# Kernel tuning notes

Hardware: AMD Instinct MI355X
Metric: run time of the kernel (lower is better)

Reference implementation:

```python
import jax, jax.numpy as jnp
import numpy as np

B, L, DIM = 1, 2048, 4096
H, KV, HD = 32, 8, 128
REP = H // KV
SCALE = HD ** -0.5
ROPE_BASE = 10000.0


def rope_traditional(x, offset=0):
    # x: [B, H, L, D] ; traditional RoPE rotates interleaved pairs (x[2i], x[2i+1])
    D = x.shape[-1]
    Lx = x.shape[2]
    pos = jnp.arange(offset, offset + Lx, dtype=jnp.float32)            # [L]
    inv_freq = ROPE_BASE ** (-jnp.arange(0, D, 2, dtype=jnp.float32) / D)  # [D/2]
    ang = pos[:, None] * inv_freq[None, :]                               # [L, D/2]
    c, s = jnp.cos(ang), jnp.sin(ang)
    x1 = x[..., 0::2]
    x2 = x[..., 1::2]
    r1 = x1 * c - x2 * s
    r2 = x1 * s + x2 * c
    return jnp.stack([r1, r2], axis=-1).reshape(x.shape).astype(x.dtype)


def setup_inputs() -> dict:
    key = jax.random.key(0)
    k0, k1, k2, k3, k4 = jax.random.split(key, 5)
    x = jax.random.normal(k0, (B, L, DIM), dtype=jnp.float32)
    wq = jax.random.normal(k1, (DIM, H * HD), dtype=jnp.float32) * 0.02
    wk = jax.random.normal(k2, (DIM, KV * HD), dtype=jnp.float32) * 0.02
    wv = jax.random.normal(k3, (DIM, KV * HD), dtype=jnp.float32) * 0.02
    wo = jax.random.normal(k4, (H * HD, DIM), dtype=jnp.float32) * 0.02
    # additive causal mask (prefill)
    causal = jnp.tril(jnp.ones((L, L), dtype=bool))
    mask = jnp.where(causal, 0.0, -1e9).astype(jnp.float32)
    return {"x": x, "wq": wq, "wk": wk, "wv": wv, "wo": wo, "mask": mask}


def reference(x, wq, wk, wv, wo, mask):
    Bx, Lx, _ = x.shape
    q = (x @ wq).reshape(Bx, Lx, H, HD).transpose(0, 2, 1, 3)   # [B,H,L,hd]
    k = (x @ wk).reshape(Bx, Lx, KV, HD).transpose(0, 2, 1, 3)  # [B,KV,L,hd]
    v = (x @ wv).reshape(Bx, Lx, KV, HD).transpose(0, 2, 1, 3)
    # GQA head repeat (each kv head repeated REP times contiguously)
    k = jnp.repeat(k, REP, axis=1)  # [B,H,L,hd]
    v = jnp.repeat(v, REP, axis=1)
    # RoPE applied after repeat (cache=None branch), offset 0
    q = rope_traditional(q)
    k = rope_traditional(k)
    scores = jnp.einsum("bhld,bhmd->bhlm", q * SCALE, k) + mask  # [B,H,L,L]
    probs = jax.nn.softmax(scores.astype(jnp.float32), axis=-1).astype(scores.dtype)
    out = jnp.einsum("bhlm,bhmd->bhld", probs, v)
    out = out.transpose(0, 2, 1, 3).reshape(Bx, Lx, H * HD)
    return out @ wo, k, v
```

## Files before the change

kernel.cpp:

```cpp
#include <hip/hip_runtime.h>
#include <hip/hip_bf16.h>
#include <math.h>


#define L_SEQ 2048
#define DIM   4096
#define NH    32
#define NKV   8
#define HD    128
#define SCALE 0.08838834764831845f

typedef __bf16 bf16x8 __attribute__((ext_vector_type(8)));
typedef __bf16 bf16x4 __attribute__((ext_vector_type(4)));
typedef __bf16 bf16x2 __attribute__((ext_vector_type(2)));
typedef float  f32x4  __attribute__((ext_vector_type(4)));

__device__ __forceinline__ void gld16(const void* g, void* l) {
  __builtin_amdgcn_global_load_lds(
      (const __attribute__((address_space(1))) void*)g,
      (__attribute__((address_space(3))) void*)l, 16, 0, 0);
}

__global__ void cast_bf16_kernel(const float* __restrict__ in,
                                 __bf16* __restrict__ out, long n4) {
  long i = blockIdx.x * (long)blockDim.x + threadIdx.x;
  if (i >= n4) return;
  float4 f = reinterpret_cast<const float4*>(in)[i];
  bf16x4 o;
  o[0] = (__bf16)f.x; o[1] = (__bf16)f.y; o[2] = (__bf16)f.z; o[3] = (__bf16)f.w;
  reinterpret_cast<bf16x4*>(out)[i] = o;
}

__global__ void tcast_kernel(const float* __restrict__ in0, __bf16* __restrict__ out0,
                             const float* __restrict__ in1, __bf16* __restrict__ out1,
                             int K, int N) {
  __shared__ float tile[32][33];
  const float* in  = blockIdx.z ? in1  : in0;
  __bf16*     out  = blockIdx.z ? out1 : out0;
  int n0 = blockIdx.x * 32, k0 = blockIdx.y * 32;
  int tx = threadIdx.x & 31, ty = threadIdx.x >> 5;
#pragma unroll
  for (int i = 0; i < 4; ++i)
    tile[ty + i * 8][tx] = in[(long)(k0 + ty + i * 8) * N + n0 + tx];
  __syncthreads();
#pragma unroll
  for (int i = 0; i < 4; ++i)
    out[(long)(n0 + ty + i * 8) * K + k0 + tx] = (__bf16)tile[tx][ty + i * 8];
}

#define GBM 128
#define GBN 256
#define ABYTES  (GBM * 64 * 2)
#define BBYTES  (GBN * 64 * 2)
#define BUFBYTES (ABYTES + BBYTES)

__global__ __launch_bounds__(512, 2) void gemm256(
    const __bf16* __restrict__ A, const __bf16* __restrict__ B0,
    const __bf16* __restrict__ B1, void* __restrict__ C0, void* __restrict__ C1,
    int M, int N, int K, int mode) {
  __shared__ char lds[3 * BUFBYTES] __attribute__((aligned(16)));
  const __bf16* Bt = blockIdx.z ? B1 : B0;
  void* C = blockIdx.z ? C1 : C0;

  const int nwg = gridDim.x * gridDim.y;
  const int bid = blockIdx.y * gridDim.x + blockIdx.x;
  const int swz = (bid & 7) * (nwg >> 3) + (bid >> 3);
  const int n0 = (swz % gridDim.x) * GBN;
  const int m0 = (swz / gridDim.x) * GBM;

  const int t = threadIdx.x, wave = t >> 6, lane = t & 63;
  const int quad = lane >> 4, l16 = lane & 15;
  const int wm = (wave >> 2) * 64, wn = (wave & 3) * 64;

  const int srow = t >> 3;
  const int scol = ((t & 7) ^ (srow & 7)) * 8;
  const __bf16* pa = A  + (long)(m0 + srow) * K + scol;
  const __bf16* pb = Bt + (long)(n0 + srow) * K + scol;
  const long K64 = (long)64 * K;
  const int ldsA = wave * 1024;
  const int ldsB = ABYTES + wave * 1024;

  int aoff[2][4], boff[2][4];
#pragma unroll
  for (int ks = 0; ks < 2; ++ks) {
    const int sw = ((ks * 4 + quad) ^ (l16 & 7)) * 16;
#pragma unroll
    for (int i = 0; i < 4; ++i) {
      aoff[ks][i] = (wm + i * 16 + l16) * 128 + sw;
      boff[ks][i] = ABYTES + (wn + i * 16 + l16) * 128 + sw;
    }
  }

  f32x4 acc[4][4] = {};
  const int nt = K >> 6;

  {
    char* bb = lds;
#pragma unroll
    for (int pt = 0; pt < 2; ++pt) {
      gld16(pa,           bb + ldsA);
      gld16(pa + K64,     bb + ldsA + 8192);
      gld16(pb,           bb + ldsB);
      gld16(pb + K64,     bb + ldsB + 8192);
      gld16(pb + 2 * K64, bb + ldsB + 16384);
      gld16(pb + 3 * K64, bb + ldsB + 24576);
      pa += 64; pb += 64;
      bb += BUFBYTES;
    }
  }

  char* cb = lds;
  char* sb = lds + 2 * BUFBYTES;

#pragma unroll 1
  for (int kt = 0; kt < nt - 1; ++kt) {
    asm volatile("s_waitcnt vmcnt(6)" ::: "memory");
    __builtin_amdgcn_s_barrier();
    bf16x8 af[4], bfr[4];
#pragma unroll
    for (int i = 0; i < 4; ++i) {
      af[i]  = *(const bf16x8*)(cb + aoff[0][i]);
      bfr[i] = *(const bf16x8*)(cb + boff[0][i]);
    }
    if (kt + 2 < nt) {
      gld16(pa,           sb + ldsA);
      gld16(pa + K64,     sb + ldsA + 8192);
      gld16(pb,           sb + ldsB);
      gld16(pb + K64,     sb + ldsB + 8192);
      gld16(pb + 2 * K64, sb + ldsB + 16384);
      gld16(pb + 3 * K64, sb + ldsB + 24576);
      pa += 64; pb += 64;
    }
    __builtin_amdgcn_s_setprio(1);
#pragma unroll
    for (int tm = 0; tm < 4; ++tm)
#pragma unroll
      for (int tn = 0; tn < 4; ++tn)
        acc[tm][tn] = __builtin_amdgcn_mfma_f32_16x16x32_bf16(
            af[tm], bfr[tn], acc[tm][tn], 0, 0, 0);
    __builtin_amdgcn_s_setprio(0);
#pragma unroll
    for (int i = 0; i < 4; ++i) {
      af[i]  = *(const bf16x8*)(cb + aoff[1][i]);
      bfr[i] = *(const bf16x8*)(cb + boff[1][i]);
    }
    __builtin_amdgcn_s_setprio(1);
#pragma unroll
    for (int tm = 0; tm < 4; ++tm)
#pragma unroll
      for (int tn = 0; tn < 4; ++tn)
        acc[tm][tn] = __builtin_amdgcn_mfma_f32_16x16x32_bf16(
            af[tm], bfr[tn], acc[tm][tn], 0, 0, 0);
    __builtin_amdgcn_s_setprio(0);
    cb += BUFBYTES; if (cb == lds + 3 * BUFBYTES) cb = lds;
    sb += BUFBYTES; if (sb == lds + 3 * BUFBYTES) sb = lds;
  }

  asm volatile("s_waitcnt vmcnt(0)" ::: "memory");
  __builtin_amdgcn_s_barrier();
  {
    bf16x8 af[4], bfr[4];
#pragma unroll
    for (int ks = 0; ks < 2; ++ks) {
#pragma unroll
      for (int i = 0; i < 4; ++i) {
        af[i]  = *(const bf16x8*)(cb + aoff[ks][i]);
        bfr[i] = *(const bf16x8*)(cb + boff[ks][i]);
      }
      __builtin_amdgcn_s_setprio(1);
#pragma unroll
      for (int tm = 0; tm < 4; ++tm)
#pragma unroll
        for (int tn = 0; tn < 4; ++tn)
          acc[tm][tn] = __builtin_amdgcn_mfma_f32_16x16x32_bf16(
              af[tm], bfr[tn], acc[tm][tn], 0, 0, 0);
      __builtin_amdgcn_s_setprio(0);
    }
  }

#pragma unroll
  for (int tm = 0; tm < 4; ++tm)
#pragma unroll
    for (int tn = 0; tn < 4; ++tn)
#pragma unroll
      for (int r = 0; r < 4; ++r) {
        int row = m0 + wm + tm * 16 + quad * 4 + r;
        int col = n0 + wn + tn * 16 + l16;
        float v = acc[tm][tn][r];
        if (mode == 0) {
          ((float*)C)[(long)row * N + col] = v;
        } else {
          long idx = ((long)(col >> 7) * L_SEQ + row) * HD + (col & 127);
          ((__bf16*)C)[idx] = (__bf16)v;
        }
      }
}

#define NLOG2_10K 13.287712379549449f

__global__ void rope_q_kernel(__bf16* __restrict__ q ) {
  int idx = blockIdx.x * blockDim.x + threadIdx.x;
  int i = idx & 63, l = (idx >> 6) & 2047, h = idx >> 17;
  if (h >= NH) return;
  long base = ((long)h * L_SEQ + l) * HD + 2 * i;
  bf16x2 x12 = *(bf16x2*)(q + base);
  float x1 = (float)x12[0], x2 = (float)x12[1];
  float inv = exp2f((float)i * (-NLOG2_10K / 64.0f));
  float s, c; __sincosf((float)l * inv, &s, &c);
  bf16x2 o; o[0] = (__bf16)(x1 * c - x2 * s); o[1] = (__bf16)(x1 * s + x2 * c);
  *(bf16x2*)(q + base) = o;
}

__global__ void ropekv_kernel(__bf16* __restrict__ kb ,
                              const __bf16* __restrict__ vb,
                              float* __restrict__ kout ,
                              float* __restrict__ vout) {
  int idx = blockIdx.x * blockDim.x + threadIdx.x;
  int i = idx & 63, l = (idx >> 6) & 2047, kv = idx >> 17;
  if (kv >= NKV) return;
  long base = ((long)kv * L_SEQ + l) * HD + 2 * i;
  bf16x2 x12 = *(bf16x2*)(kb + base);
  float x1 = (float)x12[0], x2 = (float)x12[1];
  float inv = exp2f((float)i * (-NLOG2_10K / 64.0f));
  float s, c; __sincosf((float)l * inv, &s, &c);
  float r1 = x1 * c - x2 * s, r2 = x1 * s + x2 * c;
  bf16x2 o; o[0] = (__bf16)r1; o[1] = (__bf16)r2;
  *(bf16x2*)(kb + base) = o;
  float2 kf; kf.x = r1; kf.y = r2;
  bf16x2 vv = *(const bf16x2*)(vb + base);
  float2 vf; vf.x = (float)vv[0]; vf.y = (float)vv[1];
  long off = (long)(kv * 4) * L_SEQ * HD + (long)l * HD + 2 * i;
#pragma unroll
  for (int rr = 0; rr < 4; ++rr) {
    *(float2*)(kout + off) = kf;
    *(float2*)(vout + off) = vf;
    off += (long)L_SEQ * HD;
  }
}

__global__ void vtrans_kernel(const __bf16* __restrict__ Vh, __bf16* __restrict__ Vt) {
  __shared__ __bf16 tile[64 * 65];
  int kv = blockIdx.z, lb = blockIdx.x * 64, db = blockIdx.y * 64;
  int t = threadIdx.x;
#pragma unroll
  for (int it = 0; it < 2; ++it) {
    int c = it * 256 + t, r = c >> 3, pc = c & 7;
    bf16x8 v = *(const bf16x8*)(Vh + ((long)kv * L_SEQ + lb + r) * HD + db + pc * 8);
#pragma unroll
    for (int e = 0; e < 8; ++e) tile[r * 65 + pc * 8 + e] = v[e];
  }
  __syncthreads();
#pragma unroll
  for (int it = 0; it < 2; ++it) {
    int c = it * 256 + t, r = c >> 3, pc = c & 7;
    bf16x8 v;
#pragma unroll
    for (int e = 0; e < 8; ++e) v[e] = tile[(pc * 8 + e) * 65 + r];
    *(bf16x8*)(Vt + ((long)kv * HD + db + r) * L_SEQ + lb + pc * 8) = v;
  }
}

#define PSP 72

__global__ __launch_bounds__(256) void attn3_kernel(
    const __bf16* __restrict__ Q, const __bf16* __restrict__ K,
    const __bf16* __restrict__ Vt, __bf16* __restrict__ O ) {
  __shared__ __bf16 Ks[2][64 * 128]  __attribute__((aligned(16)));
  __shared__ __bf16 Vts[2][128 * 64] __attribute__((aligned(16)));
  __shared__ __bf16 Ps[64 * PSP]     __attribute__((aligned(16)));

  const int p = blockIdx.x;
  const int h = blockIdx.y;
  const int t = threadIdx.x, wave = t >> 6, lane = t & 63;
  const int quad = lane >> 4, l16 = lane & 15;
  const int mw = wave * 16;
  const __bf16* Kh = K  + (long)(h >> 2) * L_SEQ * HD;
  const __bf16* Vh = Vt + (long)(h >> 2) * HD * L_SEQ;
  const float SL2 = SCALE * 1.44269504f;

  int kr[4], kk[4], vr[4], vk[4];
#pragma unroll
  for (int it = 0; it < 4; ++it) {
    int c = it * 256 + t;
    kr[it] = c >> 4; kk[it] = ((c & 15) ^ (kr[it] & 7)) * 8;
    vr[it] = c >> 3; vk[it] = ((c & 7)  ^ (vr[it] & 7)) * 8;
  }

#pragma unroll 1
  for (int tsel = 0; tsel < 2; ++tsel) {
    const int qb = tsel ? (31 - p) : p;
    const int l0 = qb * 64;
    const int mq = l0 + mw + l16;

    bf16x8 bq[4];
    {
      const __bf16* qrow = Q + ((long)h * L_SEQ + mq) * HD + quad * 8;
#pragma unroll
      for (int d = 0; d < 4; ++d) bq[d] = *(const bf16x8*)(qrow + d * 32);
    }

    f32x4 o_acc[8] = {};
    float m_run = -1e30f, l_run = 0.f;

    __syncthreads();
#pragma unroll
    for (int it = 0; it < 4; ++it) {
      gld16(Kh + (long)(0 + kr[it]) * HD + kk[it],
            (char*)Ks[0] + (size_t)(it * 256 + wave * 64) * 16);
      gld16(Vh + (long)vr[it] * L_SEQ + 0 + vk[it],
            (char*)Vts[0] + (size_t)(it * 256 + wave * 64) * 16);
    }

#pragma unroll 1
    for (int j = 0; j <= qb; ++j) {
      const int cur = j & 1;
      __syncthreads();
      if (j < qb) {
        const int nxt = cur ^ 1;
#pragma unroll
        for (int it = 0; it < 4; ++it) {
          gld16(Kh + (long)((j + 1) * 64 + kr[it]) * HD + kk[it],
                (char*)Ks[nxt] + (size_t)(it * 256 + wave * 64) * 16);
          gld16(Vh + (long)vr[it] * L_SEQ + (j + 1) * 64 + vk[it],
                (char*)Vts[nxt] + (size_t)(it * 256 + wave * 64) * 16);
        }
      }

      f32x4 s[4] = {};
#pragma unroll
      for (int dsi = 0; dsi < 4; ++dsi)
#pragma unroll
        for (int tn = 0; tn < 4; ++tn) {
          bf16x8 ak = *(const bf16x8*)((char*)Ks[cur] + (tn * 16 + l16) * 256 +
                                       (((dsi * 4 + quad) ^ (l16 & 7)) * 16));
          s[tn] = __builtin_amdgcn_mfma_f32_16x16x32_bf16(ak, bq[dsi], s[tn], 0, 0, 0);
        }

#pragma unroll
      for (int tn = 0; tn < 4; ++tn)
#pragma unroll
        for (int r = 0; r < 4; ++r) {
          float v = s[tn][r] * SL2;
          if (j == qb && (j * 64 + tn * 16 + quad * 4 + r) > mq) v = -3.0e38f;
          s[tn][r] = v;
        }
      float mx = -3.0e38f;
#pragma unroll
      for (int tn = 0; tn < 4; ++tn)
#pragma unroll
        for (int r = 0; r < 4; ++r) mx = fmaxf(mx, s[tn][r]);
      mx = fmaxf(mx, __shfl_xor(mx, 16, 64));
      mx = fmaxf(mx, __shfl_xor(mx, 32, 64));
      float mnew = fmaxf(m_run, mx);
      float alpha = exp2f(m_run - mnew);
      float rs = 0.f;
#pragma unroll
      for (int tn = 0; tn < 4; ++tn)
#pragma unroll
        for (int r = 0; r < 4; ++r) {
          float pe = exp2f(s[tn][r] - mnew);
          s[tn][r] = pe; rs += pe;
        }
      rs += __shfl_xor(rs, 16, 64);
      rs += __shfl_xor(rs, 32, 64);
      l_run = l_run * alpha + rs;
      m_run = mnew;

#pragma unroll
      for (int tn = 0; tn < 4; ++tn) {
        bf16x4 pv;
#pragma unroll
        for (int r = 0; r < 4; ++r) pv[r] = (__bf16)s[tn][r];
        *(bf16x4*)(&Ps[(mw + l16) * PSP + tn * 16 + quad * 4]) = pv;
      }

#pragma unroll
      for (int td = 0; td < 8; ++td)
#pragma unroll
        for (int r = 0; r < 4; ++r) o_acc[td][r] *= alpha;
#pragma unroll
      for (int ks = 0; ks < 2; ++ks) {
        bf16x8 bp = *(const bf16x8*)(&Ps[(mw + l16) * PSP + ks * 32 + quad * 8]);
#pragma unroll
        for (int td = 0; td < 8; ++td) {
          bf16x8 av = *(const bf16x8*)((char*)Vts[cur] + (td * 16 + l16) * 128 +
                                       (((ks * 4 + quad) ^ (l16 & 7)) * 16));
          o_acc[td] = __builtin_amdgcn_mfma_f32_16x16x32_bf16(av, bp, o_acc[td], 0, 0, 0);
        }
      }
    }

    float inv_l = 1.0f / l_run;
#pragma unroll
    for (int td = 0; td < 8; ++td) {
      bf16x4 ov;
#pragma unroll
      for (int r = 0; r < 4; ++r) ov[r] = (__bf16)(o_acc[td][r] * inv_l);
      *(bf16x4*)(O + (long)mq * DIM + h * HD + td * 16 + quad * 4) = ov;
    }
  }
}

extern "C" void kernel_launch(void* const* d_in, const int* in_sizes, int n_in,
                              void* d_out, int out_size, void* d_ws, size_t ws_size,
                              hipStream_t stream) {
  const float* x  = (const float*)d_in[0];
  const float* wq = (const float*)d_in[1];
  const float* wk = (const float*)d_in[2];
  const float* wv = (const float*)d_in[3];
  const float* wo = (const float*)d_in[4];

  float* out   = (float*)d_out;
  float* k_out = out + (long)L_SEQ * DIM;
  float* v_out = k_out + (long)NH * L_SEQ * HD;

  char* ws = (char*)d_ws;
  __bf16* Xb  = (__bf16*)ws; ws += (long)L_SEQ * DIM * 2;
  __bf16* Wqt = (__bf16*)ws; ws += (long)DIM * DIM * 2;
  __bf16* Wkt = (__bf16*)ws; ws += (long)DIM * (NKV * HD) * 2;
  __bf16* Wvt = (__bf16*)ws; ws += (long)DIM * (NKV * HD) * 2;
  __bf16* Wot = (__bf16*)ws; ws += (long)DIM * DIM * 2;
  __bf16* Qh  = (__bf16*)ws; ws += (long)NH * L_SEQ * HD * 2;
  __bf16* Kh  = (__bf16*)ws; ws += (long)NKV * L_SEQ * HD * 2;
  __bf16* Vh  = (__bf16*)ws; ws += (long)NKV * L_SEQ * HD * 2;
  __bf16* Vt  = (__bf16*)ws; ws += (long)NKV * HD * L_SEQ * 2;
  __bf16* Ob  = (__bf16*)ws; ws += (long)L_SEQ * DIM * 2;

  tcast_kernel<<<dim3(DIM / 32, DIM / 32, 1), 256, 0, stream>>>(wq, Wqt, wq, Wqt, DIM, DIM);
  tcast_kernel<<<dim3((NKV * HD) / 32, DIM / 32, 2), 256, 0, stream>>>(wk, Wkt, wv, Wvt, DIM, NKV * HD);
  tcast_kernel<<<dim3(DIM / 32, DIM / 32, 1), 256, 0, stream>>>(wo, Wot, wo, Wot, DIM, DIM);
  {
    long n = (long)L_SEQ * DIM;
    cast_bf16_kernel<<<dim3(n / 1024), 256, 0, stream>>>(x, Xb, n / 4);
  }
  gemm256<<<dim3(DIM / 256, L_SEQ / 128, 1), 512, 0, stream>>>(
      Xb, Wqt, Wqt, Qh, Qh, L_SEQ, DIM, DIM, 2);
  gemm256<<<dim3((NKV * HD) / 256, L_SEQ / 128, 2), 512, 0, stream>>>(
      Xb, Wkt, Wvt, Kh, Vh, L_SEQ, NKV * HD, DIM, 2);
  rope_q_kernel<<<dim3((NH * L_SEQ * 64) / 256), 256, 0, stream>>>(Qh);
  ropekv_kernel<<<dim3((NKV * L_SEQ * 64) / 256), 256, 0, stream>>>(Kh, Vh, k_out, v_out);
  vtrans_kernel<<<dim3(L_SEQ / 64, HD / 64, NKV), 256, 0, stream>>>(Vh, Vt);
  attn3_kernel<<<dim3(16, NH), 256, 0, stream>>>(Qh, Kh, Vt, Ob);
  gemm256<<<dim3(DIM / 256, L_SEQ / 128, 1), 512, 0, stream>>>(
      Ob, Wot, Wot, out, out, L_SEQ, DIM, DIM, 0);
}
```

Measured before the change: 550.1 us.

## Use 128-row query tiles, longest-first GQA-grouped scheduling, and lazy softmax rescaling

The attention kernel now gives each wave 32 query rows (two 16-row groups) sharing every loaded K/V tile, so each block covers 128 queries instead of two 64-query tiles. Blocks are ordered longest causal tile first and interleaved so heads sharing a KV group run together, to help L2 reuse and load balance. The online softmax skips rescaling the output accumulator when the running max grows by at most a threshold, which cuts per-chunk multiplies but risks larger intermediate values. Register pressure roughly doubles (launch bounds set to one block), and the grid becomes 512 uneven blocks instead of 512 balanced paired ones.

```diff
diff --git a/kernel.cpp b/kernel.cpp
--- a/kernel.cpp
+++ b/kernel.cpp
@@ -261,21 +261,24 @@
 }
 
 #define PSP 72
-
-__global__ __launch_bounds__(256) void attn3_kernel(
+#define DTHR 8.0f
+
+__global__ __launch_bounds__(256, 1) void attn4_kernel(
     const __bf16* __restrict__ Q, const __bf16* __restrict__ K,
     const __bf16* __restrict__ Vt, __bf16* __restrict__ O ) {
   __shared__ __bf16 Ks[2][64 * 128]  __attribute__((aligned(16)));
   __shared__ __bf16 Vts[2][128 * 64] __attribute__((aligned(16)));
-  __shared__ __bf16 Ps[64 * PSP]     __attribute__((aligned(16)));
-
-  const int p = blockIdx.x;
-  const int h = blockIdx.y;
+  __shared__ __bf16 Ps[128 * PSP]    __attribute__((aligned(16)));
+
+  const int b = blockIdx.x;
+  const int kvg = b & 7;
+  const int h   = kvg * 4 + ((b >> 3) & 3);
+  const int qt  = 15 - (b >> 5);
   const int t = threadIdx.x, wave = t >> 6, lane = t & 63;
   const int quad = lane >> 4, l16 = lane & 15;
-  const int mw = wave * 16;
-  const __bf16* Kh = K  + (long)(h >> 2) * L_SEQ * HD;
-  const __bf16* Vh = Vt + (long)(h >> 2) * HD * L_SEQ;
+  const int mw = wave * 32;
+  const __bf16* Kh = K  + (long)kvg * L_SEQ * HD;
+  const __bf16* Vh = Vt + (long)kvg * HD * L_SEQ;
   const float SL2 = SCALE * 1.44269504f;
 
   int kr[4], kk[4], vr[4], vk[4];
@@ -286,117 +289,132 @@
     vr[it] = c >> 3; vk[it] = ((c & 7)  ^ (vr[it] & 7)) * 8;
   }
 
+  const int nchunk = 2 * qt + 2;
+  const int jdiag  = 2 * qt;
+
+  int mq[2]; mq[0] = qt * 128 + mw + l16; mq[1] = mq[0] + 16;
+
+  bf16x8 bq[2][4];
+#pragma unroll
+  for (int g = 0; g < 2; ++g) {
+    const __bf16* qrow = Q + ((long)h * L_SEQ + mq[g]) * HD + quad * 8;
+#pragma unroll
+    for (int d = 0; d < 4; ++d) bq[g][d] = *(const bf16x8*)(qrow + d * 32);
+  }
+
+  f32x4 o_acc[2][8] = {};
+  float m_run[2] = {-1e30f, -1e30f}, l_run[2] = {0.f, 0.f};
+
+#pragma unroll
+  for (int it = 0; it < 4; ++it) {
+    gld16(Kh + (long)kr[it] * HD + kk[it],
+          (char*)Ks[0] + (size_t)(it * 256 + wave * 64) * 16);
+    gld16(Vh + (long)vr[it] * L_SEQ + vk[it],
+          (char*)Vts[0] + (size_t)(it * 256 + wave * 64) * 16);
+  }
+
 #pragma unroll 1
-  for (int tsel = 0; tsel < 2; ++tsel) {
-    const int qb = tsel ? (31 - p) : p;
-    const int l0 = qb * 64;
-    const int mq = l0 + mw + l16;
-
-    bf16x8 bq[4];
-    {
-      const __bf16* qrow = Q + ((long)h * L_SEQ + mq) * HD + quad * 8;
-#pragma unroll
-      for (int d = 0; d < 4; ++d) bq[d] = *(const bf16x8*)(qrow + d * 32);
-    }
-
-    f32x4 o_acc[8] = {};
-    float m_run = -1e30f, l_run = 0.f;
-
+  for (int j = 0; j < nchunk; ++j) {
+    const int cur = j & 1;
     __syncthreads();
-#pragma unroll
-    for (int it = 0; it < 4; ++it) {
-      gld16(Kh + (long)(0 + kr[it]) * HD + kk[it],
-            (char*)Ks[0] + (size_t)(it * 256 + wave * 64) * 16);
-      gld16(Vh + (long)vr[it] * L_SEQ + 0 + vk[it],
-            (char*)Vts[0] + (size_t)(it * 256 + wave * 64) * 16);
-    }
-
-#pragma unroll 1
-    for (int j = 0; j <= qb; ++j) {
-      const int cur = j & 1;
-      __syncthreads();
-      if (j < qb) {
-        const int nxt = cur ^ 1;
-#pragma unroll
-        for (int it = 0; it < 4; ++it) {
-          gld16(Kh + (long)((j + 1) * 64 + kr[it]) * HD + kk[it],
-                (char*)Ks[nxt] + (size_t)(it * 256 + wave * 64) * 16);
-          gld16(Vh + (long)vr[it] * L_SEQ + (j + 1) * 64 + vk[it],
-                (char*)Vts[nxt] + (size_t)(it * 256 + wave * 64) * 16);
-        }
-      }
-
-      f32x4 s[4] = {};
-#pragma unroll
-      for (int dsi = 0; dsi < 4; ++dsi)
-#pragma unroll
-        for (int tn = 0; tn < 4; ++tn) {
-          bf16x8 ak = *(const bf16x8*)((char*)Ks[cur] + (tn * 16 + l16) * 256 +
-                                       (((dsi * 4 + quad) ^ (l16 & 7)) * 16));
-          s[tn] = __builtin_amdgcn_mfma_f32_16x16x32_bf16(ak, bq[dsi], s[tn], 0, 0, 0);
-        }
-
+    if (j + 1 < nchunk) {
+      const int nxt = cur ^ 1;
+#pragma unroll
+      for (int it = 0; it < 4; ++it) {
+        gld16(Kh + (long)((j + 1) * 64 + kr[it]) * HD + kk[it],
+              (char*)Ks[nxt] + (size_t)(it * 256 + wave * 64) * 16);
+        gld16(Vh + (long)vr[it] * L_SEQ + (j + 1) * 64 + vk[it],
+              (char*)Vts[nxt] + (size_t)(it * 256 + wave * 64) * 16);
+      }
+    }
+
+    f32x4 s[2][4] = {};
+#pragma unroll
+    for (int dsi = 0; dsi < 4; ++dsi)
+#pragma unroll
+      for (int tn = 0; tn < 4; ++tn) {
+        bf16x8 ak = *(const bf16x8*)((char*)Ks[cur] + (tn * 16 + l16) * 256 +
+                                     (((dsi * 4 + quad) ^ (l16 & 7)) * 16));
+        s[0][tn] = __builtin_amdgcn_mfma_f32_16x16x32_bf16(ak, bq[0][dsi], s[0][tn], 0, 0, 0);
+        s[1][tn] = __builtin_amdgcn_mfma_f32_16x16x32_bf16(ak, bq[1][dsi], s[1][tn], 0, 0, 0);
+      }
+
+#pragma unroll
+    for (int g = 0; g < 2; ++g) {
 #pragma unroll
       for (int tn = 0; tn < 4; ++tn)
 #pragma unroll
         for (int r = 0; r < 4; ++r) {
-          float v = s[tn][r] * SL2;
-          if (j == qb && (j * 64 + tn * 16 + quad * 4 + r) > mq) v = -3.0e38f;
-          s[tn][r] = v;
+          float v = s[g][tn][r] * SL2;
+          if (j >= jdiag && (j * 64 + tn * 16 + quad * 4 + r) > mq[g]) v = -3.0e38f;
+          s[g][tn][r] = v;
         }
       float mx = -3.0e38f;
 #pragma unroll
       for (int tn = 0; tn < 4; ++tn)
 #pragma unroll
-        for (int r = 0; r < 4; ++r) mx = fmaxf(mx, s[tn][r]);
+        for (int r = 0; r < 4; ++r) mx = fmaxf(mx, s[g][tn][r]);
       mx = fmaxf(mx, __shfl_xor(mx, 16, 64));
       mx = fmaxf(mx, __shfl_xor(mx, 32, 64));
-      float mnew = fmaxf(m_run, mx);
-      float alpha = exp2f(m_run - mnew);
+
+      const bool defer = __all(mx - m_run[g] <= DTHR);
+      const float mnew = defer ? m_run[g] : fmaxf(m_run[g], mx);
+
       float rs = 0.f;
 #pragma unroll
       for (int tn = 0; tn < 4; ++tn)
 #pragma unroll
         for (int r = 0; r < 4; ++r) {
-          float pe = exp2f(s[tn][r] - mnew);
-          s[tn][r] = pe; rs += pe;
+          float pe = exp2f(s[g][tn][r] - mnew);
+          s[g][tn][r] = pe; rs += pe;
         }
       rs += __shfl_xor(rs, 16, 64);
       rs += __shfl_xor(rs, 32, 64);
-      l_run = l_run * alpha + rs;
-      m_run = mnew;
+
+      if (defer) {
+        l_run[g] += rs;
+      } else {
+        float alpha = exp2f(m_run[g] - mnew);
+#pragma unroll
+        for (int td = 0; td < 8; ++td)
+#pragma unroll
+          for (int r = 0; r < 4; ++r) o_acc[g][td][r] *= alpha;
+        l_run[g] = l_run[g] * alpha + rs;
+        m_run[g] = mnew;
+      }
 
 #pragma unroll
       for (int tn = 0; tn < 4; ++tn) {
         bf16x4 pv;
 #pragma unroll
-        for (int r = 0; r < 4; ++r) pv[r] = (__bf16)s[tn][r];
-        *(bf16x4*)(&Ps[(mw + l16) * PSP + tn * 16 + quad * 4]) = pv;
-      }
-
-#pragma unroll
-      for (int td = 0; td < 8; ++td)
-#pragma unroll
-        for (int r = 0; r < 4; ++r) o_acc[td][r] *= alpha;
-#pragma unroll
-      for (int ks = 0; ks < 2; ++ks) {
-        bf16x8 bp = *(const bf16x8*)(&Ps[(mw + l16) * PSP + ks * 32 + quad * 8]);
-#pragma unroll
-        for (int td = 0; td < 8; ++td) {
-          bf16x8 av = *(const bf16x8*)((char*)Vts[cur] + (td * 16 + l16) * 128 +
-                                       (((ks * 4 + quad) ^ (l16 & 7)) * 16));
-          o_acc[td] = __builtin_amdgcn_mfma_f32_16x16x32_bf16(av, bp, o_acc[td], 0, 0, 0);
-        }
-      }
-    }
-
-    float inv_l = 1.0f / l_run;
+        for (int r = 0; r < 4; ++r) pv[r] = (__bf16)s[g][tn][r];
+        *(bf16x4*)(&Ps[(mw + g * 16 + l16) * PSP + tn * 16 + quad * 4]) = pv;
+      }
+    }
+
+#pragma unroll
+    for (int ks = 0; ks < 2; ++ks) {
+      bf16x8 bp0 = *(const bf16x8*)(&Ps[(mw + l16) * PSP + ks * 32 + quad * 8]);
+      bf16x8 bp1 = *(const bf16x8*)(&Ps[(mw + 16 + l16) * PSP + ks * 32 + quad * 8]);
+#pragma unroll
+      for (int td = 0; td < 8; ++td) {
+        bf16x8 av = *(const bf16x8*)((char*)Vts[cur] + (td * 16 + l16) * 128 +
+                                     (((ks * 4 + quad) ^ (l16 & 7)) * 16));
+        o_acc[0][td] = __builtin_amdgcn_mfma_f32_16x16x32_bf16(av, bp0, o_acc[0][td], 0, 0, 0);
+        o_acc[1][td] = __builtin_amdgcn_mfma_f32_16x16x32_bf16(av, bp1, o_acc[1][td], 0, 0, 0);
+      }
+    }
+  }
+
+#pragma unroll
+  for (int g = 0; g < 2; ++g) {
+    float inv_l = 1.0f / l_run[g];
 #pragma unroll
     for (int td = 0; td < 8; ++td) {
       bf16x4 ov;
 #pragma unroll
-      for (int r = 0; r < 4; ++r) ov[r] = (__bf16)(o_acc[td][r] * inv_l);
-      *(bf16x4*)(O + (long)mq * DIM + h * HD + td * 16 + quad * 4) = ov;
+      for (int r = 0; r < 4; ++r) ov[r] = (__bf16)(o_acc[g][td][r] * inv_l);
+      *(bf16x4*)(O + (long)mq[g] * DIM + h * HD + td * 16 + quad * 4) = ov;
     }
   }
 }
@@ -440,7 +458,7 @@
   rope_q_kernel<<<dim3((NH * L_SEQ * 64) / 256), 256, 0, stream>>>(Qh);
   ropekv_kernel<<<dim3((NKV * L_SEQ * 64) / 256), 256, 0, stream>>>(Kh, Vh, k_out, v_out);
   vtrans_kernel<<<dim3(L_SEQ / 64, HD / 64, NKV), 256, 0, stream>>>(Vh, Vt);
-  attn3_kernel<<<dim3(16, NH), 256, 0, stream>>>(Qh, Kh, Vt, Ob);
+  attn4_kernel<<<dim3(512), 256, 0, stream>>>(Qh, Kh, Vt, Ob);
   gemm256<<<dim3(DIM / 256, L_SEQ / 128, 1), 512, 0, stream>>>(
       Ob, Wot, Wot, out, out, L_SEQ, DIM, DIM, 0);
 }
```

After: 572.1 us. 1.04x slower.
